# Optimization experiments

Hardware: AMD Instinct MI355X
Metric: run time of the kernel (lower is better)

Reference implementation:

```python
import jax, jax.numpy as jnp
import numpy as np


def _ln(x, g, b):
    m = x.mean(-1, keepdims=True)
    v = ((x - m) ** 2).mean(-1, keepdims=True)
    return (x - m) * jax.lax.rsqrt(v + 1e-5) * g + b


def _forward(x, fx_in, pre_w1, pre_b1, pre_w2, pre_b2, placeholder,
             ln1_g, ln1_b, px_w, px_b, pfx_w, pfx_b, slice_w, slice_b, temp,
             q_w, k_w, v_w, out_w, out_b, ln2_g, ln2_b,
             mlp_w1, mlp_b1, mlp_w2, mlp_b2,
             ln3_g, ln3_b, head_w1, head_b1, head_w2, head_b2):
    # All linear weights are stored as [in, out] (pre-transposed vs torch nn.Linear).
    B, N, _ = x.shape
    L, H = temp.shape
    dh = slice_w.shape[1]
    gelu = lambda t: jax.nn.gelu(t, approximate=False)
    # preprocess MLP (n_layers=0, res=False): Linear -> GELU -> Linear
    h = jnp.concatenate([x, fx_in], axis=-1)
    h = gelu(h @ pre_w1 + pre_b1) @ pre_w2 + pre_b2
    h = h + placeholder  # learned [D] offset
    scale = 1.0 / jnp.sqrt(jnp.asarray(dh, h.dtype))
    for i in range(L):  # loop over structurally distinct layers
        y = _ln(h, ln1_g[i], ln1_b[i])
        # project to per-head features: bhnd
        fx_mid = (y @ pfx_w[i] + pfx_b[i]).reshape(B, N, H, dh).transpose(0, 2, 1, 3)
        x_mid = (y @ px_w[i] + px_b[i]).reshape(B, N, H, dh).transpose(0, 2, 1, 3)
        # soft slice assignment over G slices
        logits = jnp.einsum('bhnd,dg->bhng', x_mid, slice_w[i]) + slice_b[i]
        sw = jax.nn.softmax(logits / temp[i][None, :, None, None], axis=-1)  # bhng
        norm = sw.sum(axis=2)  # bhg
        tok = jnp.einsum('bhnd,bhng->bhgd', fx_mid, sw) / (norm + 1e-5)[..., None]
        # attention over G=slice_num tokens
        q = tok @ q_w[i]
        k = tok @ k_w[i]
        v = tok @ v_w[i]
        attn = jax.nn.softmax(jnp.einsum('bhgd,bhmd->bhgm', q, k) * scale, axis=-1)
        out_slice = jnp.einsum('bhgm,bhmd->bhgd', attn, v)
        # deslice back to points
        out_x = jnp.einsum('bhgd,bhng->bhnd', out_slice, sw)
        out_x = out_x.transpose(0, 2, 1, 3).reshape(B, N, H * dh)
        h = h + (out_x @ out_w[i] + out_b[i])
        z = _ln(h, ln2_g[i], ln2_b[i])
        h = h + (gelu(z @ mlp_w1[i] + mlp_b1[i]) @ mlp_w2[i] + mlp_b2[i])
    z = _ln(h, ln3_g, ln3_b)
    return gelu(z @ head_w1 + head_b1) @ head_w2 + head_b2


def setup_inputs() -> dict:
    key = jax.random.key(0)
    B, N, D, H, dh, G, L = 2, 16384, 256, 8, 32, 64, 5
    SP, FUN, OUT = 2, 4, 4
    ID = H * dh  # inner_dim == n_hidden
    MR = D * 1   # mlp_ratio=1
    ks = iter(jax.random.split(key, 64))
    nrm = lambda shape, s=0.02: jax.random.normal(next(ks), shape, jnp.float32) * s
    return dict(
        x=jax.random.normal(next(ks), (B, N, SP), jnp.float32),
        fx_in=jax.random.normal(next(ks), (B, N, FUN), jnp.float32),
        pre_w1=nrm((SP + FUN, 2 * D)), pre_b1=jnp.zeros((2 * D,), jnp.float32),
        pre_w2=nrm((2 * D, D)), pre_b2=jnp.zeros((D,), jnp.float32),
        placeholder=nrm((D,)),
        ln1_g=jnp.ones((L, D), jnp.float32), ln1_b=jnp.zeros((L, D), jnp.float32),
        px_w=nrm((L, D, ID)), px_b=jnp.zeros((L, ID), jnp.float32),
        pfx_w=nrm((L, D, ID)), pfx_b=jnp.zeros((L, ID), jnp.float32),
        slice_w=nrm((L, dh, G), 0.1), slice_b=jnp.zeros((L, G), jnp.float32),
        temp=0.5 * jnp.ones((L, H), jnp.float32),
        q_w=nrm((L, dh, dh), 0.1), k_w=nrm((L, dh, dh), 0.1), v_w=nrm((L, dh, dh), 0.1),
        out_w=nrm((L, ID, D)), out_b=jnp.zeros((L, D), jnp.float32),
        ln2_g=jnp.ones((L, D), jnp.float32), ln2_b=jnp.zeros((L, D), jnp.float32),
        mlp_w1=nrm((L, D, MR)), mlp_b1=jnp.zeros((L, MR), jnp.float32),
        mlp_w2=nrm((L, MR, D)), mlp_b2=jnp.zeros((L, D), jnp.float32),
        ln3_g=jnp.ones((D,), jnp.float32), ln3_b=jnp.zeros((D,), jnp.float32),
        head_w1=nrm((D, D)), head_b1=jnp.zeros((D,), jnp.float32),
        head_w2=nrm((D, OUT)), head_b2=jnp.zeros((OUT,), jnp.float32),
    )


def reference(x, fx_in, pre_w1, pre_b1, pre_w2, pre_b2, placeholder,
              ln1_g, ln1_b, px_w, px_b, pfx_w, pfx_b, slice_w, slice_b, temp,
              q_w, k_w, v_w, out_w, out_b, ln2_g, ln2_b,
              mlp_w1, mlp_b1, mlp_w2, mlp_b2,
              ln3_g, ln3_b, head_w1, head_b1, head_w2, head_b2):
    return _forward(x, fx_in, pre_w1, pre_b1, pre_w2, pre_b2, placeholder,
                    ln1_g, ln1_b, px_w, px_b, pfx_w, pfx_b, slice_w, slice_b, temp,
                    q_w, k_w, v_w, out_w, out_b, ln2_g, ln2_b,
                    mlp_w1, mlp_b1, mlp_w2, mlp_b2,
                    ln3_g, ln3_b, head_w1, head_b1, head_w2, head_b2)
```

## Files before the change

kernel.cpp:

```cpp
#include <hip/hip_runtime.h>


#define MTOK 32768
#define NB   16384

typedef unsigned short u16;
using short8 = __attribute__((ext_vector_type(8))) short;
using f4     = __attribute__((ext_vector_type(4))) float;

__device__ __forceinline__ float bfu(u16 u) {
    return __uint_as_float(((unsigned)u) << 16);
}
__device__ __forceinline__ u16 f2bf(float f) {
    unsigned u = __float_as_uint(f);
    u += 0x7FFFu + ((u >> 16) & 1u);
    return (u16)(u >> 16);
}
__device__ __forceinline__ float ldf(const void* p, int i, int isbf) {
    return isbf ? bfu(((const u16*)p)[i]) : ((const float*)p)[i];
}
__device__ __forceinline__ float4 dec4(ushort4 u) {
    return make_float4(bfu(u.x), bfu(u.y), bfu(u.z), bfu(u.w));
}
__device__ __forceinline__ float gelu_f(float x) {
    return 0.5f * x * (1.0f + erff(x * 0.7071067811865475f));
}

#define F_H      ((size_t)0)
#define F_OS     ((size_t)8388608)
#define F_TOKP   ((size_t)8421376)
#define F_NORMP  ((size_t)10518528)
#define F_TOK    ((size_t)10584064)
#define F_NORM   ((size_t)10616832)
#define F_BIAS   ((size_t)10617856)
#define F_PARAMS ((size_t)10626048)
#define F_BF     ((size_t)10858884)
#define B_PB2C 0
#define B_OUTB 256
#define B_M1B  1536
#define B_M2B  2816
#define B_HB1  4096
#define B_SP   4352
#define B_END  8192
#define U_WT     ((size_t)0)
#define WT_PRE2  0
#define WT_HEAD1 131072
#define WT_SPFX  196608
#define WT_OUT   1179648
#define WT_MLP1  1507328
#define WT_MLP2  1835008
#define WT_END   2162688
#define U_Y   ((size_t)2162688)
#define U_XM  ((size_t)10551296)
#define U_FM  ((size_t)18939904)
#define U_SW  ((size_t)27328512)

#define P_X    0
#define P_FX   65536
#define P_W1   196608
#define P_B1   199680
#define P_LN1G 200192
#define P_LN1B 201472
#define P_LN2G 202752
#define P_LN2B 204032
#define P_LN3G 205312
#define P_LN3B 205568
#define P_SLW  205824
#define P_SLB  216064
#define P_TEMP 216384
#define P_QW   216448
#define P_KW   221568
#define P_VW   226688
#define P_HW2  231808
#define P_HB2  232832
#define P_END  232836

__global__ __launch_bounds__(256) void cvt_kernel(
    const void* x, const void* fx, const void* w1, const void* b1,
    const void* l1g, const void* l1b, const void* l2g, const void* l2b,
    const void* l3g, const void* l3b, const void* slw, const void* slb,
    const void* tmp, const void* qw, const void* kw, const void* vw,
    const void* hw2, const void* hb2, float* __restrict__ P)
{
    int isbf = (((const u16*)tmp)[0] != 0);
    int idx = blockIdx.x * 256 + threadIdx.x;
    const void* s; int o;
    if      (idx < 65536)  { s = x;   o = idx; }
    else if (idx < 196608) { s = fx;  o = idx - 65536; }
    else if (idx < 199680) { s = w1;  o = idx - 196608; }
    else if (idx < 200192) { s = b1;  o = idx - 199680; }
    else if (idx < 201472) { s = l1g; o = idx - 200192; }
    else if (idx < 202752) { s = l1b; o = idx - 201472; }
    else if (idx < 204032) { s = l2g; o = idx - 202752; }
    else if (idx < 205312) { s = l2b; o = idx - 204032; }
    else if (idx < 205568) { s = l3g; o = idx - 205312; }
    else if (idx < 205824) { s = l3b; o = idx - 205568; }
    else if (idx < 216064) { s = slw; o = idx - 205824; }
    else if (idx < 216384) { s = slb; o = idx - 216064; }
    else if (idx < 216424) { s = tmp; o = idx - 216384; }
    else if (idx < 216448) { return; }
    else if (idx < 221568) { s = qw;  o = idx - 216448; }
    else if (idx < 226688) { s = kw;  o = idx - 221568; }
    else if (idx < 231808) { s = vw;  o = idx - 226688; }
    else if (idx < 232832) { s = hw2; o = idx - 231808; }
    else if (idx < 232836) { s = hb2; o = idx - 232832; }
    else return;
    P[idx] = ldf(s, o, isbf);
}

__global__ __launch_bounds__(256) void prep_main(
    const void* pre_w2, const void* head_w1, const void* pfx_w,
    const void* out_w, const void* mlp_w1, const void* mlp_w2,
    const void* pre_b2, const void* placeholder, const void* pfx_b,
    const void* out_b, const void* mlp_b1, const void* mlp_b2,
    const void* head_b1, const void* tmp,
    u16* __restrict__ WT, float* __restrict__ BIAS)
{
    int isbf = (((const u16*)tmp)[0] != 0);
    int idx = blockIdx.x * 256 + threadIdx.x;
    if (idx < 131072) {
        int n = idx >> 9, k = idx & 511;
        WT[WT_PRE2 + idx] = f2bf(ldf(pre_w2, k * 256 + n, isbf));
    } else if (idx < 196608) {
        int f = idx - 131072;
        int n = f >> 8, k = f & 255;
        WT[WT_HEAD1 + f] = f2bf(ldf(head_w1, k * 256 + n, isbf));
    } else if (idx < 524288) {
        int f = idx - 196608;
        int i = f >> 16, r = f & 65535;
        int n = r >> 8, k = r & 255;
        WT[WT_SPFX + (size_t)i * 196608 + (512 + n) * 256 + k] =
            f2bf(ldf(pfx_w, i * 65536 + k * 256 + n, isbf));
    } else if (idx < 1507328) {
        int f = idx - 524288;
        int mat = f >> 16, r = f & 65535;
        const void* s; int off = (mat % 5) * 65536;
        if      (mat < 5)  s = out_w;
        else if (mat < 10) s = mlp_w1;
        else               s = mlp_w2;
        int n = r >> 8, k = r & 255;
        WT[WT_OUT + f] = f2bf(ldf(s, off + k * 256 + n, isbf));
    } else if (idx < 1507584) {
        int c = idx - 1507328;
        BIAS[B_PB2C + c] = ldf(pre_b2, c, isbf) + ldf(placeholder, c, isbf);
    } else if (idx < 1508864) {
        int o = idx - 1507584; BIAS[B_OUTB + o] = ldf(out_b, o, isbf);
    } else if (idx < 1510144) {
        int o = idx - 1508864; BIAS[B_M1B + o] = ldf(mlp_b1, o, isbf);
    } else if (idx < 1511424) {
        int o = idx - 1510144; BIAS[B_M2B + o] = ldf(mlp_b2, o, isbf);
    } else if (idx < 1511680) {
        int o = idx - 1511424; BIAS[B_HB1 + o] = ldf(head_b1, o, isbf);
    } else if (idx < 1512960) {
        int o = idx - 1511680;
        int i = o >> 8, c = o & 255;
        BIAS[B_SP + i * 768 + 512 + c] = ldf(pfx_b, o, isbf);
    }
}

__global__ __launch_bounds__(256) void prep_pxsl(
    const void* px_w, const void* px_b, const void* slw, const void* slb,
    const void* tmp, u16* __restrict__ WT, float* __restrict__ BIAS)
{
    int isbf = (((const u16*)tmp)[0] != 0);
    __shared__ float pxs[64 * 33];
    __shared__ float sls[2048];
    int blk = blockIdx.x;
    int i = blk >> 5, h = (blk >> 2) & 7, kb = blk & 3;
    int t = threadIdx.x;
#pragma unroll
    for (int p = 0; p < 8; ++p) {
        int flat = t + 256 * p;
        sls[flat] = ldf(slw, i * 2048 + flat, isbf);
        int k = flat >> 5, d = flat & 31;
        pxs[k * 33 + d] = ldf(px_w, i * 65536 + (kb * 64 + k) * 256 + h * 32 + d, isbf);
    }
    __syncthreads();
    int k = t & 63, gb = t >> 6;
    float acc[16];
#pragma unroll
    for (int gi = 0; gi < 16; ++gi) acc[gi] = 0.f;
#pragma unroll
    for (int d = 0; d < 32; ++d) {
        float pv = pxs[k * 33 + d];
        const float* sp = sls + d * 64 + gb * 16;
#pragma unroll
        for (int gi = 0; gi < 16; ++gi) acc[gi] = fmaf(pv, sp[gi], acc[gi]);
    }
    u16* WTp = WT + WT_SPFX + (size_t)i * 196608;
#pragma unroll
    for (int gi = 0; gi < 16; ++gi) {
        int n = h * 64 + gb * 16 + gi;
        WTp[n * 256 + kb * 64 + k] = f2bf(acc[gi]);
    }
    if (kb == 0 && t < 64) {
        int g = t;
        float a = ldf(slb, i * 64 + g, isbf);
#pragma unroll
        for (int d = 0; d < 32; ++d)
            a = fmaf(ldf(px_b, i * 256 + h * 32 + d, isbf), sls[d * 64 + g], a);
        BIAS[B_SP + i * 768 + h * 64 + g] = a;
    }
}

__global__ __launch_bounds__(256) void pre1_kernel(
    const float* __restrict__ P, u16* __restrict__ HID)
{
    __shared__ float w1s[3072];
    __shared__ float b1s[512];
    int t = threadIdx.x;
#pragma unroll
    for (int p = 0; p < 12; ++p) w1s[t + 256 * p] = P[P_W1 + t + 256 * p];
    b1s[t] = P[P_B1 + t];
    b1s[t + 256] = P[P_B1 + t + 256];
    __syncthreads();
    int m = blockIdx.x * 4 + (t >> 6);
    int j0 = (t & 63) * 8;
    float xa = P[P_X + m * 2],     xb = P[P_X + m * 2 + 1];
    float fa = P[P_FX + m * 4],    fb = P[P_FX + m * 4 + 1];
    float fc = P[P_FX + m * 4 + 2], fd = P[P_FX + m * 4 + 3];
    u16 o[8];
#pragma unroll
    for (int jj = 0; jj < 8; ++jj) {
        int j = j0 + jj;
        float a = b1s[j];
        a = fmaf(xa, w1s[j], a);
        a = fmaf(xb, w1s[512 + j], a);
        a = fmaf(fa, w1s[1024 + j], a);
        a = fmaf(fb, w1s[1536 + j], a);
        a = fmaf(fc, w1s[2048 + j], a);
        a = fmaf(fd, w1s[2560 + j], a);
        o[jj] = f2bf(gelu_f(a));
    }
    size_t base = (size_t)m * 512 + j0;
    *(ushort4*)(HID + base)     = make_ushort4(o[0], o[1], o[2], o[3]);
    *(ushort4*)(HID + base + 4) = make_ushort4(o[4], o[5], o[6], o[7]);
}

template <int KK, int OMODE>
__global__ __launch_bounds__(256, 4) void gemm_mfma(
    const u16* __restrict__ A, const u16* __restrict__ Wt,
    const float* __restrict__ bias, float* __restrict__ C, u16* __restrict__ Cb)
{
    __shared__ u16 As[128 * 64];
    __shared__ u16 Bs[128 * 64];
    const int t = threadIdx.x;
    const int wave = t >> 6, lane = t & 63;
    const int quad = lane >> 4, l15 = lane & 15;
    const int m0 = blockIdx.x * 128;
    const int n0 = blockIdx.y * 128;
    const int wm = (wave & 1) * 64, wn = (wave >> 1) * 64;
    f4 acc[4][4];
#pragma unroll
    for (int i = 0; i < 4; ++i)
#pragma unroll
        for (int j = 0; j < 4; ++j) acc[i][j] = (f4){0.f, 0.f, 0.f, 0.f};

    for (int kc = 0; kc < KK; kc += 64) {
        if (kc) __syncthreads();
#pragma unroll
        for (int p = 0; p < 4; ++p) {
            int c = t + 256 * p;
            int row = c >> 3, c8 = c & 7;
            int off = row * 64 + ((c8 ^ (row & 7)) << 3);
            *(ulonglong2*)(As + off) =
                *(const ulonglong2*)(A + (size_t)(m0 + row) * KK + kc + c8 * 8);
            *(ulonglong2*)(Bs + off) =
                *(const ulonglong2*)(Wt + (size_t)(n0 + row) * KK + kc + c8 * 8);
        }
        __syncthreads();
#pragma unroll
        for (int kk = 0; kk < 2; ++kk) {
            short8 a[4], b[4];
#pragma unroll
            for (int i = 0; i < 4; ++i) {
                int R = wm + i * 16 + l15;
                a[i] = *(const short8*)(As + R * 64 + (((quad + kk * 4) ^ (R & 7)) << 3));
            }
#pragma unroll
            for (int j = 0; j < 4; ++j) {
                int R = wn + j * 16 + l15;
                b[j] = *(const short8*)(Bs + R * 64 + (((quad + kk * 4) ^ (R & 7)) << 3));
            }
#pragma unroll
            for (int i = 0; i < 4; ++i)
#pragma unroll
                for (int j = 0; j < 4; ++j)
                    acc[i][j] = __builtin_amdgcn_mfma_f32_16x16x32_bf16(
                        a[i], b[j], acc[i][j], 0, 0, 0);
        }
    }
#pragma unroll
    for (int j = 0; j < 4; ++j) {
        int cj = n0 + wn + j * 16 + l15;
        float bj = bias[cj];
#pragma unroll
        for (int i = 0; i < 4; ++i) {
            int rbase = m0 + wm + i * 16 + quad * 4;
#pragma unroll
            for (int r = 0; r < 4; ++r) {
                float v = acc[i][j][r] + bj;
                size_t off = (size_t)(rbase + r) * 256 + cj;
                if (OMODE == 3) v = gelu_f(v);
                if (OMODE == 1) v += C[off];
                if (OMODE >= 2) Cb[off] = f2bf(v);
                else            C[off] = v;
            }
        }
    }
}

__global__ __launch_bounds__(256, 4) void gemm_spfx(
    const u16* __restrict__ A, const u16* __restrict__ Wt,
    const float* __restrict__ bsp, const float* __restrict__ tempv,
    u16* __restrict__ SW, u16* __restrict__ FM)
{
    __shared__ u16 As[128 * 64];
    __shared__ u16 Bs[128 * 64];
    const int t = threadIdx.x;
    const int wave = t >> 6, lane = t & 63;
    const int quad = lane >> 4, l15 = lane & 15;
    const int m0 = blockIdx.x * 128;
    const int n0 = blockIdx.y * 128;
    const int wm = (wave & 1) * 64, wn = (wave >> 1) * 64;
    f4 acc[4][4];
#pragma unroll
    for (int i = 0; i < 4; ++i)
#pragma unroll
        for (int j = 0; j < 4; ++j) acc[i][j] = (f4){0.f, 0.f, 0.f, 0.f};

    for (int kc = 0; kc < 256; kc += 64) {
        if (kc) __syncthreads();
#pragma unroll
        for (int p = 0; p < 4; ++p) {
            int c = t + 256 * p;
            int row = c >> 3, c8 = c & 7;
            int off = row * 64 + ((c8 ^ (row & 7)) << 3);
            *(ulonglong2*)(As + off) =
                *(const ulonglong2*)(A + (size_t)(m0 + row) * 256 + kc + c8 * 8);
            *(ulonglong2*)(Bs + off) =
                *(const ulonglong2*)(Wt + (size_t)(n0 + row) * 256 + kc + c8 * 8);
        }
        __syncthreads();
#pragma unroll
        for (int kk = 0; kk < 2; ++kk) {
            short8 a[4], b[4];
#pragma unroll
            for (int i = 0; i < 4; ++i) {
                int R = wm + i * 16 + l15;
                a[i] = *(const short8*)(As + R * 64 + (((quad + kk * 4) ^ (R & 7)) << 3));
            }
#pragma unroll
            for (int j = 0; j < 4; ++j) {
                int R = wn + j * 16 + l15;
                b[j] = *(const short8*)(Bs + R * 64 + (((quad + kk * 4) ^ (R & 7)) << 3));
            }
#pragma unroll
            for (int i = 0; i < 4; ++i)
#pragma unroll
                for (int j = 0; j < 4; ++j)
                    acc[i][j] = __builtin_amdgcn_mfma_f32_16x16x32_bf16(
                        a[i], b[j], acc[i][j], 0, 0, 0);
        }
    }
    float bj[4];
#pragma unroll
    for (int j = 0; j < 4; ++j) bj[j] = bsp[n0 + wn + j * 16 + l15];
    if (blockIdx.y < 4) {
        const int h = (n0 + wn) >> 6;
        const float itemp = 1.0f / tempv[h];
#pragma unroll
        for (int i = 0; i < 4; ++i) {
#pragma unroll
            for (int r = 0; r < 4; ++r) {
                float v[4];
                float mx = -3.0e38f;
#pragma unroll
                for (int j = 0; j < 4; ++j) {
                    v[j] = (acc[i][j][r] + bj[j]) * itemp;
                    mx = fmaxf(mx, v[j]);
                }
#pragma unroll
                for (int o = 1; o < 16; o <<= 1) mx = fmaxf(mx, __shfl_xor(mx, o));
                float s = 0.f;
#pragma unroll
                for (int j = 0; j < 4; ++j) { v[j] = expf(v[j] - mx); s += v[j]; }
#pragma unroll
                for (int o = 1; o < 16; o <<= 1) s += __shfl_xor(s, o);
                float inv = 1.0f / s;
                int m = m0 + wm + i * 16 + quad * 4 + r;
                int b = m >> 14, n = m & 16383;
                size_t base = (((size_t)(b * 8 + h)) * NB + n) * 64;
#pragma unroll
                for (int j = 0; j < 4; ++j)
                    SW[base + j * 16 + l15] = f2bf(v[j] * inv);
            }
        }
    } else {
        int cj = (n0 - 512) + wn + l15;
#pragma unroll
        for (int j = 0; j < 4; ++j) {
            int col = cj + j * 16;
#pragma unroll
            for (int i = 0; i < 4; ++i) {
                int rbase = m0 + wm + i * 16 + quad * 4;
#pragma unroll
                for (int r = 0; r < 4; ++r)
                    FM[(size_t)(rbase + r) * 256 + col] = f2bf(acc[i][j][r] + bj[j]);
            }
        }
    }
}

__global__ __launch_bounds__(256) void ln_kernel(
    const float* __restrict__ X, const float* __restrict__ g,
    const float* __restrict__ b, u16* __restrict__ Y)
{
    int lane = threadIdx.x & 63;
    size_t m = (size_t)blockIdx.x * 4 + (threadIdx.x >> 6);
    const float4 x4 = *(const float4*)(X + m * 256 + lane * 4);
    float s = x4.x + x4.y + x4.z + x4.w;
    float q = x4.x * x4.x + x4.y * x4.y + x4.z * x4.z + x4.w * x4.w;
#pragma unroll
    for (int o = 32; o; o >>= 1) { s += __shfl_xor(s, o); q += __shfl_xor(q, o); }
    float mean = s * (1.0f / 256.0f);
    float var = q * (1.0f / 256.0f) - mean * mean;
    float inv = 1.0f / sqrtf(var + 1e-5f);
    const float4 g4 = *(const float4*)(g + lane * 4);
    const float4 b4 = *(const float4*)(b + lane * 4);
    ushort4 y;
    y.x = f2bf((x4.x - mean) * inv * g4.x + b4.x);
    y.y = f2bf((x4.y - mean) * inv * g4.y + b4.y);
    y.z = f2bf((x4.z - mean) * inv * g4.z + b4.z);
    y.w = f2bf((x4.w - mean) * inv * g4.w + b4.w);
    *(ushort4*)(Y + m * 256 + lane * 4) = y;
}

__global__ __launch_bounds__(256) void tok1_kernel(
    const u16* __restrict__ FM, const u16* __restrict__ SW,
    float* __restrict__ TOKP, float* __restrict__ NORMP)
{
    int bh = blockIdx.x >> 6, chunk = blockIdx.x & 63;
    int b = bh >> 3, hd = bh & 7;
    int t = threadIdx.x, wave = t >> 6, lane = t & 63;
    int g0 = (lane >> 3) * 8, d0 = (lane & 7) * 4;
    float4 acc[8];
#pragma unroll
    for (int gi = 0; gi < 8; ++gi) acc[gi] = make_float4(0.f, 0.f, 0.f, 0.f);
    float4 n0a = make_float4(0.f, 0.f, 0.f, 0.f);
    float4 n1a = make_float4(0.f, 0.f, 0.f, 0.f);
    int nbase = chunk * 256 + wave * 64;
    const u16* fmB = FM + ((size_t)b * NB + nbase) * 256 + hd * 32 + d0;
    const u16* swB = SW + ((size_t)bh * NB + nbase) * 64 + g0;
    for (int j = 0; j < 64; ++j) {
        float4 f4v = dec4(*(const ushort4*)(fmB + (size_t)j * 256));
        float4 s0 = dec4(*(const ushort4*)(swB + (size_t)j * 64));
        float4 s1 = dec4(*(const ushort4*)(swB + (size_t)j * 64 + 4));
#define TOKACC(gi, sv)                                            \
        acc[gi].x = fmaf(f4v.x, sv, acc[gi].x);                   \
        acc[gi].y = fmaf(f4v.y, sv, acc[gi].y);                   \
        acc[gi].z = fmaf(f4v.z, sv, acc[gi].z);                   \
        acc[gi].w = fmaf(f4v.w, sv, acc[gi].w);
        TOKACC(0, s0.x) TOKACC(1, s0.y) TOKACC(2, s0.z) TOKACC(3, s0.w)
        TOKACC(4, s1.x) TOKACC(5, s1.y) TOKACC(6, s1.z) TOKACC(7, s1.w)
#undef TOKACC
        n0a.x += s0.x; n0a.y += s0.y; n0a.z += s0.z; n0a.w += s0.w;
        n1a.x += s1.x; n1a.y += s1.y; n1a.z += s1.z; n1a.w += s1.w;
    }
    __shared__ float red[4][2048];
    __shared__ float nred[4][64];
#pragma unroll
    for (int gi = 0; gi < 8; ++gi)
        *(float4*)&red[wave][(g0 + gi) * 32 + d0] = acc[gi];
    if ((lane & 7) == 0) {
        nred[wave][g0 + 0] = n0a.x; nred[wave][g0 + 1] = n0a.y;
        nred[wave][g0 + 2] = n0a.z; nred[wave][g0 + 3] = n0a.w;
        nred[wave][g0 + 4] = n1a.x; nred[wave][g0 + 5] = n1a.y;
        nred[wave][g0 + 6] = n1a.z; nred[wave][g0 + 7] = n1a.w;
    }
    __syncthreads();
    size_t tokBase = (size_t)(chunk * 16 + bh) * 2048;
#pragma unroll
    for (int k = 0; k < 8; ++k) {
        int c = t + 256 * k;
        TOKP[tokBase + c] = red[0][c] + red[1][c] + red[2][c] + red[3][c];
    }
    if (t < 64)
        NORMP[(chunk * 16 + bh) * 64 + t] = nred[0][t] + nred[1][t] + nred[2][t] + nred[3][t];
}

__global__ __launch_bounds__(256) void tok2_kernel(
    const float* __restrict__ TOKP, const float* __restrict__ NORMP,
    float* __restrict__ TOK, float* __restrict__ NORM)
{
    int idx = blockIdx.x * 256 + threadIdx.x;
    if (idx < 32768) {
        int bh = idx >> 11, c = idx & 2047;
        float s = 0.f;
#pragma unroll 8
        for (int ch = 0; ch < 64; ++ch) s += TOKP[(size_t)(ch * 16 + bh) * 2048 + c];
        TOK[idx] = s;
    } else if (idx < 33792) {
        int o = idx - 32768;
        int bh = o >> 6, g = o & 63;
        float s = 0.f;
#pragma unroll 8
        for (int ch = 0; ch < 64; ++ch) s += NORMP[(ch * 16 + bh) * 64 + g];
        NORM[o] = s;
    }
}

__global__ __launch_bounds__(256) void attn_kernel(
    const float* __restrict__ TOK, const float* __restrict__ NORM,
    const float* __restrict__ qw, const float* __restrict__ kw,
    const float* __restrict__ vw, float* __restrict__ OS)
{
    __shared__ float tokd[2048], qs[2048], ks[2048], vs[2048];
    int bh = blockIdx.x;
    int t = threadIdx.x;
#pragma unroll
    for (int i = 0; i < 2; ++i) {
        int f4v = t + 256 * i;
        float4 v = *(const float4*)(TOK + (size_t)bh * 2048 + f4v * 4);
        float inv = 1.0f / (NORM[bh * 64 + (f4v >> 3)] + 1e-5f);
        v.x *= inv; v.y *= inv; v.z *= inv; v.w *= inv;
        *(float4*)&tokd[f4v * 4] = v;
    }
    __syncthreads();
#pragma unroll
    for (int i = 0; i < 8; ++i) {
        int f = t + 256 * i;
        int g = f >> 5, d = f & 31;
        const float* tr = tokd + g * 32;
        float aq = 0.f, ak = 0.f, av = 0.f;
#pragma unroll
        for (int e = 0; e < 32; ++e) {
            float tv = tr[e];
            aq = fmaf(tv, qw[e * 32 + d], aq);
            ak = fmaf(tv, kw[e * 32 + d], ak);
            av = fmaf(tv, vw[e * 32 + d], av);
        }
        qs[f] = aq; ks[f] = ak; vs[f] = av;
    }
    __syncthreads();
    int g = t >> 2, sub = t & 3;
    float4 qv[8];
#pragma unroll
    for (int e4 = 0; e4 < 8; ++e4) qv[e4] = *(const float4*)(qs + g * 32 + e4 * 4);
    float p[16];
    float mx = -3.0e38f;
#pragma unroll
    for (int mm = 0; mm < 16; ++mm) {
        int mI = sub * 16 + mm;
        const float4* kr = (const float4*)(ks + mI * 32);
        float s = 0.f;
#pragma unroll
        for (int e4 = 0; e4 < 8; ++e4) {
            float4 kv = kr[e4];
            s = fmaf(qv[e4].x, kv.x, s); s = fmaf(qv[e4].y, kv.y, s);
            s = fmaf(qv[e4].z, kv.z, s); s = fmaf(qv[e4].w, kv.w, s);
        }
        s *= 0.17677669529663687f;
        p[mm] = s;
        mx = fmaxf(mx, s);
    }
    mx = fmaxf(mx, __shfl_xor(mx, 1));
    mx = fmaxf(mx, __shfl_xor(mx, 2));
    float lsum = 0.f;
#pragma unroll
    for (int mm = 0; mm < 16; ++mm) { p[mm] = expf(p[mm] - mx); lsum += p[mm]; }
    lsum += __shfl_xor(lsum, 1);
    lsum += __shfl_xor(lsum, 2);
    float inv = 1.0f / lsum;
    float4 oa[8];
#pragma unroll
    for (int d4 = 0; d4 < 8; ++d4) oa[d4] = make_float4(0.f, 0.f, 0.f, 0.f);
#pragma unroll
    for (int mm = 0; mm < 16; ++mm) {
        int mI = sub * 16 + mm;
        const float4* vr = (const float4*)(vs + mI * 32);
        float pm = p[mm];
#pragma unroll
        for (int d4 = 0; d4 < 8; ++d4) {
            float4 vv = vr[d4];
            oa[d4].x = fmaf(pm, vv.x, oa[d4].x);
            oa[d4].y = fmaf(pm, vv.y, oa[d4].y);
            oa[d4].z = fmaf(pm, vv.z, oa[d4].z);
            oa[d4].w = fmaf(pm, vv.w, oa[d4].w);
        }
    }
#pragma unroll
    for (int d4 = 0; d4 < 8; ++d4) {
        oa[d4].x += __shfl_xor(oa[d4].x, 1); oa[d4].x += __shfl_xor(oa[d4].x, 2);
        oa[d4].y += __shfl_xor(oa[d4].y, 1); oa[d4].y += __shfl_xor(oa[d4].y, 2);
        oa[d4].z += __shfl_xor(oa[d4].z, 1); oa[d4].z += __shfl_xor(oa[d4].z, 2);
        oa[d4].w += __shfl_xor(oa[d4].w, 1); oa[d4].w += __shfl_xor(oa[d4].w, 2);
    }
    float4 r0 = oa[sub * 2], r1 = oa[sub * 2 + 1];
    r0.x *= inv; r0.y *= inv; r0.z *= inv; r0.w *= inv;
    r1.x *= inv; r1.y *= inv; r1.z *= inv; r1.w *= inv;
    *(float4*)(OS + (size_t)bh * 2048 + g * 32 + sub * 8)     = r0;
    *(float4*)(OS + (size_t)bh * 2048 + g * 32 + sub * 8 + 4) = r1;
}

__global__ __launch_bounds__(256) void deslice_kernel(
    const float* __restrict__ OS, const u16* __restrict__ SW, u16* __restrict__ OX)
{
    __shared__ float swt[8 * 16 * 64];
    int blk = blockIdx.x;
    int b = blk >> 10, n0 = (blk & 1023) * 16;
    int t = threadIdx.x;
    int hd = t >> 5, d = t & 31;
#pragma unroll
    for (int i = 0; i < 8; ++i) {
        int f4v = t + 256 * i;
        int hd2 = f4v >> 8, mm = (f4v >> 4) & 15, g4 = f4v & 15;
        ushort4 u = *(const ushort4*)(SW + (((size_t)(b * 8 + hd2)) * NB + n0 + mm) * 64 + g4 * 4);
        *(float4*)&swt[(hd2 * 16 + mm) * 64 + g4 * 4] = dec4(u);
    }
    __syncthreads();
    float acc[16];
#pragma unroll
    for (int mm = 0; mm < 16; ++mm) acc[mm] = 0.f;
    const float* osb = OS + ((size_t)(b * 8 + hd)) * 2048 + d;
#pragma unroll 4
    for (int g4 = 0; g4 < 16; ++g4) {
        float o0 = osb[(g4 * 4 + 0) * 32], o1 = osb[(g4 * 4 + 1) * 32];
        float o2 = osb[(g4 * 4 + 2) * 32], o3 = osb[(g4 * 4 + 3) * 32];
        const float* swp = swt + hd * 1024 + g4 * 4;
#pragma unroll
        for (int mm = 0; mm < 16; ++mm) {
            float4 sv = *(const float4*)(swp + mm * 64);
            acc[mm] = fmaf(o0, sv.x, fmaf(o1, sv.y, fmaf(o2, sv.z, fmaf(o3, sv.w, acc[mm]))));
        }
    }
#pragma unroll
    for (int mm = 0; mm < 16; ++mm)
        OX[((size_t)b * NB + n0 + mm) * 256 + t] = f2bf(acc[mm]);
}

__global__ __launch_bounds__(256) void head2_kernel(
    const u16* __restrict__ HID, const float* __restrict__ w2,
    const float* __restrict__ b2, const void* tmp, void* __restrict__ OUT)
{
    int isbf = (((const u16*)tmp)[0] != 0);
    int lane = threadIdx.x & 63;
    size_t m = (size_t)blockIdx.x * 4 + (threadIdx.x >> 6);
    const float4 hv = dec4(*(const ushort4*)(HID + m * 256 + lane * 4));
    float4 a = make_float4(0.f, 0.f, 0.f, 0.f);
    float hcomp[4] = {hv.x, hv.y, hv.z, hv.w};
#pragma unroll
    for (int i = 0; i < 4; ++i) {
        const float4 wv = *(const float4*)(w2 + (lane * 4 + i) * 4);
        float h = hcomp[i];
        a.x = fmaf(h, wv.x, a.x); a.y = fmaf(h, wv.y, a.y);
        a.z = fmaf(h, wv.z, a.z); a.w = fmaf(h, wv.w, a.w);
    }
#pragma unroll
    for (int o = 32; o; o >>= 1) {
        a.x += __shfl_xor(a.x, o); a.y += __shfl_xor(a.y, o);
        a.z += __shfl_xor(a.z, o); a.w += __shfl_xor(a.w, o);
    }
    if (lane == 0) {
        float o0 = a.x + b2[0], o1 = a.y + b2[1], o2 = a.z + b2[2], o3 = a.w + b2[3];
        if (isbf) {
            ushort4 r; r.x = f2bf(o0); r.y = f2bf(o1); r.z = f2bf(o2); r.w = f2bf(o3);
            *(ushort4*)((u16*)OUT + m * 4) = r;
        } else {
            *(float4*)((float*)OUT + m * 4) = make_float4(o0, o1, o2, o3);
        }
    }
}

extern "C" void kernel_launch(void* const* d_in, const int* in_sizes, int n_in,
                              void* d_out, int out_size, void* d_ws, size_t ws_size,
                              hipStream_t stream)
{
    const void* x = d_in[0];      const void* fx = d_in[1];
    const void* pre_w1 = d_in[2]; const void* pre_b1 = d_in[3];
    const void* pre_w2 = d_in[4]; const void* pre_b2 = d_in[5];
    const void* placeholder = d_in[6];
    const void* ln1_g = d_in[7];  const void* ln1_b = d_in[8];
    const void* px_w = d_in[9];   const void* px_b = d_in[10];
    const void* pfx_w = d_in[11]; const void* pfx_b = d_in[12];
    const void* slice_w = d_in[13]; const void* slice_b = d_in[14];
    const void* temp = d_in[15];
    const void* q_w = d_in[16];   const void* k_w = d_in[17]; const void* v_w = d_in[18];
    const void* out_w = d_in[19]; const void* out_b = d_in[20];
    const void* ln2_g = d_in[21]; const void* ln2_b = d_in[22];
    const void* mlp_w1 = d_in[23]; const void* mlp_b1 = d_in[24];
    const void* mlp_w2 = d_in[25]; const void* mlp_b2 = d_in[26];
    const void* ln3_g = d_in[27]; const void* ln3_b = d_in[28];
    const void* head_w1 = d_in[29]; const void* head_b1 = d_in[30];
    const void* head_w2 = d_in[31]; const void* head_b2 = d_in[32];

    float* ws = (float*)d_ws;
    float* H     = ws + F_H;
    float* OSp   = ws + F_OS;
    float* TOKP  = ws + F_TOKP;
    float* NORMP = ws + F_NORMP;
    float* TOKf  = ws + F_TOK;
    float* NORMf = ws + F_NORM;
    float* BIAS  = ws + F_BIAS;
    float* P     = ws + F_PARAMS;
    u16*   U     = (u16*)(ws + F_BF);
    u16*   WT    = U + U_WT;
    u16*   Yb    = U + U_Y;
    u16*   XMb   = U + U_XM;
    u16*   FMb   = U + U_FM;
    u16*   SWb   = U + U_SW;
    u16*   HIDb  = U + U_XM;

    cvt_kernel<<<910, 256, 0, stream>>>(x, fx, pre_w1, pre_b1, ln1_g, ln1_b,
        ln2_g, ln2_b, ln3_g, ln3_b, slice_w, slice_b, temp, q_w, k_w, v_w,
        head_w2, head_b2, P);
    prep_main<<<5910, 256, 0, stream>>>(pre_w2, head_w1, pfx_w, out_w, mlp_w1,
        mlp_w2, pre_b2, placeholder, pfx_b, out_b, mlp_b1, mlp_b2, head_b1,
        temp, WT, BIAS);
    prep_pxsl<<<160, 256, 0, stream>>>(px_w, px_b, slice_w, slice_b, temp, WT, BIAS);
    pre1_kernel<<<8192, 256, 0, stream>>>(P, HIDb);

    dim3 gg(256, 2);
    dim3 gsp(256, 6);
    gemm_mfma<512, 0><<<gg, 256, 0, stream>>>(HIDb, WT + WT_PRE2, BIAS + B_PB2C, H, nullptr);

    for (int i = 0; i < 5; ++i) {
        ln_kernel<<<8192, 256, 0, stream>>>(H, P + P_LN1G + i * 256, P + P_LN1B + i * 256, Yb);
        gemm_spfx<<<gsp, 256, 0, stream>>>(Yb, WT + WT_SPFX + (size_t)i * 196608,
            BIAS + B_SP + i * 768, P + P_TEMP + i * 8, SWb, FMb);
        tok1_kernel<<<1024, 256, 0, stream>>>(FMb, SWb, TOKP, NORMP);
        tok2_kernel<<<132, 256, 0, stream>>>(TOKP, NORMP, TOKf, NORMf);
        attn_kernel<<<16, 256, 0, stream>>>(TOKf, NORMf, P + P_QW + i * 1024,
            P + P_KW + i * 1024, P + P_VW + i * 1024, OSp);
        deslice_kernel<<<2048, 256, 0, stream>>>(OSp, SWb, Yb);
        gemm_mfma<256, 1><<<gg, 256, 0, stream>>>(Yb, WT + WT_OUT + i * 65536,
            BIAS + B_OUTB + i * 256, H, nullptr);
        ln_kernel<<<8192, 256, 0, stream>>>(H, P + P_LN2G + i * 256, P + P_LN2B + i * 256, Yb);
        gemm_mfma<256, 3><<<gg, 256, 0, stream>>>(Yb, WT + WT_MLP1 + i * 65536,
            BIAS + B_M1B + i * 256, nullptr, XMb);
        gemm_mfma<256, 1><<<gg, 256, 0, stream>>>(XMb, WT + WT_MLP2 + i * 65536,
            BIAS + B_M2B + i * 256, H, nullptr);
    }

    ln_kernel<<<8192, 256, 0, stream>>>(H, P + P_LN3G, P + P_LN3B, Yb);
    gemm_mfma<256, 3><<<gg, 256, 0, stream>>>(Yb, WT + WT_HEAD1, BIAS + B_HB1, nullptr, XMb);
    head2_kernel<<<8192, 256, 0, stream>>>(XMb, P + P_HW2, P + P_HB2, temp, d_out);
}
```

Measured before the change: 1.229 ms.

## Load GEMM tiles directly into LDS with global_load_lds and coalesce pre1 stores

```diff
diff --git a/kernel.cpp b/kernel.cpp
--- a/kernel.cpp
+++ b/kernel.cpp
@@ -24,6 +24,12 @@
 }
 __device__ __forceinline__ float gelu_f(float x) {
     return 0.5f * x * (1.0f + erff(x * 0.7071067811865475f));
+}
+
+typedef __attribute__((address_space(1))) const unsigned int* as1p;
+typedef __attribute__((address_space(3))) unsigned int* as3p;
+__device__ __forceinline__ void gload_lds16(const u16* g, u16* l) {
+    __builtin_amdgcn_global_load_lds((as1p)g, (as3p)l, 16, 0, 0);
 }
 
 #define F_H      ((size_t)0)
@@ -215,14 +221,14 @@
     b1s[t + 256] = P[P_B1 + t + 256];
     __syncthreads();
     int m = blockIdx.x * 4 + (t >> 6);
-    int j0 = (t & 63) * 8;
-    float xa = P[P_X + m * 2],     xb = P[P_X + m * 2 + 1];
-    float fa = P[P_FX + m * 4],    fb = P[P_FX + m * 4 + 1];
+    int lane = t & 63;
+    float xa = P[P_X + m * 2],      xb = P[P_X + m * 2 + 1];
+    float fa = P[P_FX + m * 4],     fb = P[P_FX + m * 4 + 1];
     float fc = P[P_FX + m * 4 + 2], fd = P[P_FX + m * 4 + 3];
-    u16 o[8];
+    size_t base = (size_t)m * 512 + lane;
 #pragma unroll
     for (int jj = 0; jj < 8; ++jj) {
-        int j = j0 + jj;
+        int j = lane + 64 * jj;
         float a = b1s[j];
         a = fmaf(xa, w1s[j], a);
         a = fmaf(xb, w1s[512 + j], a);
@@ -230,11 +236,8 @@
         a = fmaf(fb, w1s[1536 + j], a);
         a = fmaf(fc, w1s[2048 + j], a);
         a = fmaf(fd, w1s[2560 + j], a);
-        o[jj] = f2bf(gelu_f(a));
-    }
-    size_t base = (size_t)m * 512 + j0;
-    *(ushort4*)(HID + base)     = make_ushort4(o[0], o[1], o[2], o[3]);
-    *(ushort4*)(HID + base + 4) = make_ushort4(o[4], o[5], o[6], o[7]);
+        HID[base + 64 * jj] = f2bf(gelu_f(a));
+    }
 }
 
 template <int KK, int OMODE>
@@ -250,6 +253,8 @@
     const int m0 = blockIdx.x * 128;
     const int n0 = blockIdx.y * 128;
     const int wm = (wave & 1) * 64, wn = (wave >> 1) * 64;
+    const int r0 = wave * 32;
+    const int lrow = lane >> 3, ls = lane & 7;
     f4 acc[4][4];
 #pragma unroll
     for (int i = 0; i < 4; ++i)
@@ -259,14 +264,13 @@
     for (int kc = 0; kc < KK; kc += 64) {
         if (kc) __syncthreads();
 #pragma unroll
-        for (int p = 0; p < 4; ++p) {
-            int c = t + 256 * p;
-            int row = c >> 3, c8 = c & 7;
-            int off = row * 64 + ((c8 ^ (row & 7)) << 3);
-            *(ulonglong2*)(As + off) =
-                *(const ulonglong2*)(A + (size_t)(m0 + row) * KK + kc + c8 * 8);
-            *(ulonglong2*)(Bs + off) =
-                *(const ulonglong2*)(Wt + (size_t)(n0 + row) * KK + kc + c8 * 8);
+        for (int q = 0; q < 4; ++q) {
+            int row = r0 + q * 8 + lrow;
+            int chunk = ls ^ (row & 7);
+            gload_lds16(A  + (size_t)(m0 + row) * KK + kc + chunk * 8,
+                        As + (r0 + q * 8) * 64);
+            gload_lds16(Wt + (size_t)(n0 + row) * KK + kc + chunk * 8,
+                        Bs + (r0 + q * 8) * 64);
         }
         __syncthreads();
 #pragma unroll
@@ -323,6 +327,8 @@
     const int m0 = blockIdx.x * 128;
     const int n0 = blockIdx.y * 128;
     const int wm = (wave & 1) * 64, wn = (wave >> 1) * 64;
+    const int r0 = wave * 32;
+    const int lrow = lane >> 3, ls = lane & 7;
     f4 acc[4][4];
 #pragma unroll
     for (int i = 0; i < 4; ++i)
@@ -332,14 +338,13 @@
     for (int kc = 0; kc < 256; kc += 64) {
         if (kc) __syncthreads();
 #pragma unroll
-        for (int p = 0; p < 4; ++p) {
-            int c = t + 256 * p;
-            int row = c >> 3, c8 = c & 7;
-            int off = row * 64 + ((c8 ^ (row & 7)) << 3);
-            *(ulonglong2*)(As + off) =
-                *(const ulonglong2*)(A + (size_t)(m0 + row) * 256 + kc + c8 * 8);
-            *(ulonglong2*)(Bs + off) =
-                *(const ulonglong2*)(Wt + (size_t)(n0 + row) * 256 + kc + c8 * 8);
+        for (int q = 0; q < 4; ++q) {
+            int row = r0 + q * 8 + lrow;
+            int chunk = ls ^ (row & 7);
+            gload_lds16(A  + (size_t)(m0 + row) * 256 + kc + chunk * 8,
+                        As + (r0 + q * 8) * 64);
+            gload_lds16(Wt + (size_t)(n0 + row) * 256 + kc + chunk * 8,
+                        Bs + (r0 + q * 8) * 64);
         }
         __syncthreads();
 #pragma unroll
```

After: 1.164 ms. 1.06x faster.
